# Kernel optimization log

Hardware: AMD Instinct MI355X
Metric: run time of the kernel (lower is better)

The kernel has to match this reference:

```python
import jax, jax.numpy as jnp
import numpy as np

NUM_EMBEDDINGS = 1024
EMBEDDING_DIM = 256

def setup_inputs() -> dict:
    key = jax.random.key(0)
    k1, k2 = jax.random.split(key)
    z_e = jax.random.normal(k1, (32, 256, 64, 64), dtype=jnp.float32)
    # nn.Embedding weight init uniform_(-1/K, 1/K)
    lim = 1.0 / NUM_EMBEDDINGS
    codebook = jax.random.uniform(k2, (NUM_EMBEDDINGS, EMBEDDING_DIM), dtype=jnp.float32,
                                  minval=-lim, maxval=lim)
    return {"z_e": z_e, "codebook": codebook}

def reference(z_e, codebook):
    B, C, H, W = z_e.shape
    # [B,C,H,W] -> [B*H*W, C]
    z_flat = jnp.transpose(z_e, (0, 2, 3, 1)).reshape(-1, C)
    # squared L2 distances: ||z||^2 + ||e||^2 - 2 z.e  -> [N, K]
    distances = (jnp.sum(z_flat ** 2, axis=1, keepdims=True)
                 + jnp.sum(codebook ** 2, axis=1)
                 - 2.0 * jnp.matmul(z_flat, codebook.T))
    encoding_indices = jnp.argmin(distances, axis=1)  # [N]
    z_q = codebook[encoding_indices].reshape(B, H, W, C)
    z_q = jnp.transpose(z_q, (0, 3, 1, 2))  # [B,C,H,W]
    sg = jax.lax.stop_gradient
    codebook_loss = jnp.mean((sg(z_q) - z_e) ** 2)
    commitment_loss = jnp.mean((sg(z_e) - z_q) ** 2)
    return z_q, codebook_loss + 0.25 * commitment_loss, encoding_indices
```

## Files before the change

kernel.cpp:

```cpp
#include <hip/hip_runtime.h>
#include <stdint.h>

typedef __attribute__((ext_vector_type(8))) _Float16 half8;
typedef __attribute__((ext_vector_type(4))) float f32x4;

#define CDIM 256
#define KCODES 1024
#define NPTS 131072
#define ZQ_ELEMS 33554432u
#define CAP 32768
#define MARGIN 3.0e-4f

#define WS_IMG 0
#define WS_S2 (16 * 65536)
#define WS_IDX (WS_S2 + 4096)
#define WS_PART (WS_IDX + NPTS * 4)
#define WS_CNT (WS_PART + 65536)
#define WS_LIST (WS_CNT + 64)

__device__ __forceinline__ float np_pairwise_sq_256(const float* x) {
    float res[2];
#pragma unroll
    for (int h = 0; h < 2; h++) {
        const float* a = x + h * 128;
        float r[8];
#pragma unroll
        for (int j = 0; j < 8; j++) r[j] = __fmul_rn(a[j], a[j]);
#pragma unroll
        for (int i = 8; i < 128; i += 8)
#pragma unroll
            for (int j = 0; j < 8; j++)
                r[j] = __fadd_rn(r[j], __fmul_rn(a[i + j], a[i + j]));
        res[h] = __fadd_rn(__fadd_rn(__fadd_rn(r[0], r[1]), __fadd_rn(r[2], r[3])),
                           __fadd_rn(__fadd_rn(r[4], r[5]), __fadd_rn(r[6], r[7])));
    }
    return __fadd_rn(res[0], res[1]);
}

__global__ __launch_bounds__(256) void vq_prepall(const float* __restrict__ cb,
                                                  unsigned char* __restrict__ img,
                                                  float* __restrict__ s2,
                                                  float* __restrict__ cbT,
                                                  int* __restrict__ cnt) {
    __shared__ float rows[32 * 261];
    int t = threadIdx.x;
    int k0 = blockIdx.x * 32;
    if (blockIdx.x == 0 && t == 0) *cnt = 0;
#pragma unroll
    for (int i = 0; i < 8; i++) {
        int u = i * 256 + t;
        int row = u >> 6, c4 = u & 63;
        float4 v = *(const float4*)&cb[(size_t)(k0 + row) * CDIM + c4 * 4];
        float* d = &rows[row * 261 + c4 * 4];
        d[0] = v.x; d[1] = v.y; d[2] = v.z; d[3] = v.w;
    }
    __syncthreads();
    if (t < 32) s2[k0 + t] = np_pairwise_sq_256(&rows[t * 261]);
#pragma unroll
    for (int i = 0; i < 4; i++) {
        int u = i * 256 + t;
        int cl = u >> 5, cg = u & 31;
        union H { _Float16 h[8]; uint4 u4; } hv;
#pragma unroll
        for (int j = 0; j < 8; j++) hv.h[j] = (_Float16)(rows[cl * 261 + cg * 8 + j] * 1024.f);
        int ks = cg >> 2, l4 = cg & 3;
        int q = cl >> 4, l15 = cl & 15;
        int lane = l4 * 16 + l15;
        *(uint4*)(img + (size_t)blockIdx.x * 16384 + ((ks * 2 + q) << 10) + lane * 16) = hv.u4;
    }
#pragma unroll
    for (int i = 0; i < 32; i++) {
        int u = i * 256 + t;
        int c = u >> 5, row = u & 31;
        cbT[(size_t)c * 1024 + k0 + row] = rows[row * 261 + c];
    }
}

__global__ __launch_bounds__(256, 2) void vq_dist(const float* __restrict__ z,
                                                  const unsigned char* __restrict__ img,
                                                  const float* __restrict__ s2g,
                                                  int* __restrict__ outIdx,
                                                  int* __restrict__ cnt,
                                                  int* __restrict__ list,
                                                  float* __restrict__ partial) {
    __shared__ __align__(16) unsigned char smem[3][16384];
    __shared__ float e2s[1024];
    __shared__ float lred[4];
    int t = threadIdx.x;
    int lane = t & 63, wave = t >> 6;
    int l15 = lane & 15, l4 = lane >> 4;
    int blk0 = blockIdx.x * 256;
    int wbase = blk0 + wave * 64;
    int b = blk0 >> 12;
    int hwb0 = blk0 & 4095;
    const float* zb = z + (size_t)b * (CDIM * 4096);
    unsigned char* sbase = &smem[0][0];

#pragma unroll
    for (int i = 0; i < 4; i++) e2s[t + i * 256] = s2g[t + i * 256];

    half8 aHi[4][8];
    float s1p[4] = {0.f, 0.f, 0.f, 0.f};
#pragma unroll
    for (int ks = 0; ks < 8; ks++) {
        __syncthreads();
#pragma unroll
        for (int i = 0; i < 8; i++) {
            int u = i * 256 + t;
            int row = u >> 6, col16 = u & 63;
            const float* gsrc = zb + (size_t)(ks * 32 + row) * 4096 + hwb0 + col16 * 4;
            __builtin_amdgcn_global_load_lds(
                (const __attribute__((address_space(1))) void*)gsrc,
                (__attribute__((address_space(3))) void*)(sbase + (size_t)u * 16), 16, 0, 0);
        }
        __syncthreads();
#pragma unroll
        for (int m = 0; m < 4; m++) {
            half8 h;
            float ss = s1p[m];
#pragma unroll
            for (int j = 0; j < 8; j++) {
                float f = *(const float*)(sbase +
                        (size_t)(((l4 * 8 + j) << 8) + wave * 64 + m * 16 + l15) * 4) * 32.f;
                h[j] = (_Float16)f;
                ss = fmaf(f, f, ss);
            }
            aHi[m][ks] = h;
            s1p[m] = ss;
        }
    }
    __syncthreads();
#pragma unroll
    for (int m = 0; m < 4; m++) {
        s1p[m] += __shfl_xor(s1p[m], 16);
        s1p[m] += __shfl_xor(s1p[m], 32);
    }

#pragma unroll
    for (int i = 0; i < 4; i++) {
        size_t off = (size_t)(i * 256 + t) * 16;
        __builtin_amdgcn_global_load_lds(
            (const __attribute__((address_space(1))) void*)(img + off),
            (__attribute__((address_space(3))) void*)(&smem[0][0] + off), 16, 0, 0);
    }
#pragma unroll
    for (int i = 0; i < 4; i++) {
        size_t off = (size_t)(i * 256 + t) * 16;
        __builtin_amdgcn_global_load_lds(
            (const __attribute__((address_space(1))) void*)(img + 16384 + off),
            (__attribute__((address_space(3))) void*)(&smem[1][0] + off), 16, 0, 0);
    }

    float bestv[4][4], bestv2[4][4];
    int besti[4][4];
#pragma unroll
    for (int m = 0; m < 4; m++)
#pragma unroll
        for (int j = 0; j < 4; j++) { bestv[m][j] = 3.0e38f; bestv2[m][j] = 3.0e38f; besti[m][j] = 0; }

    int i0 = 0, i1 = 1, i2 = 2;
    for (int chunk = 0; chunk < 32; chunk++) {
        if (chunk < 31) asm volatile("s_waitcnt vmcnt(4)" ::: "memory");
        else            asm volatile("s_waitcnt vmcnt(0)" ::: "memory");
        __builtin_amdgcn_s_barrier();

        if (chunk + 2 < 32) {
            const unsigned char* src = img + (size_t)(chunk + 2) * 16384;
            unsigned char* dst = &smem[0][0] + (size_t)i2 * 16384;
#pragma unroll
            for (int i = 0; i < 4; i++) {
                size_t off = (size_t)(i * 256 + t) * 16;
                __builtin_amdgcn_global_load_lds(
                    (const __attribute__((address_space(1))) void*)(src + off),
                    (__attribute__((address_space(3))) void*)(dst + off), 16, 0, 0);
            }
        }

        f32x4 acc[4][2];
#pragma unroll
        for (int m = 0; m < 4; m++)
#pragma unroll
            for (int q = 0; q < 2; q++) acc[m][q] = (f32x4){0.f, 0.f, 0.f, 0.f};

        const unsigned char* bufc = &smem[0][0] + (size_t)i0 * 16384 + lane * 16;
#pragma unroll
        for (int ks = 0; ks < 8; ks++) {
            half8 b0 = *(const half8*)(bufc + (ks << 11));
            half8 b1 = *(const half8*)(bufc + (ks << 11) + 1024);
#pragma unroll
            for (int m = 0; m < 4; m++) {
                acc[m][0] = __builtin_amdgcn_mfma_f32_16x16x32_f16(aHi[m][ks], b0, acc[m][0], 0, 0, 0);
                acc[m][1] = __builtin_amdgcn_mfma_f32_16x16x32_f16(aHi[m][ks], b1, acc[m][1], 0, 0, 0);
            }
        }
#pragma unroll
        for (int q = 0; q < 2; q++) {
            int code = chunk * 32 + q * 16 + l15;
            float ev = e2s[code];
#pragma unroll
            for (int m = 0; m < 4; m++)
#pragma unroll
                for (int j = 0; j < 4; j++) {
                    float s = fmaf(acc[m][q][j], -6.103515625e-05f, ev);
                    if (s < bestv[m][j]) { bestv2[m][j] = bestv[m][j]; bestv[m][j] = s; besti[m][j] = code; }
                    else if (s < bestv2[m][j]) bestv2[m][j] = s;
                }
        }
        int tmp = i0; i0 = i1; i1 = i2; i2 = tmp;
    }

    float lsum = 0.f;
#pragma unroll
    for (int m = 0; m < 4; m++)
#pragma unroll
        for (int j = 0; j < 4; j++) {
            float v = bestv[m][j], v2 = bestv2[m][j];
            int idx = besti[m][j];
#pragma unroll
            for (int off = 1; off < 16; off <<= 1) {
                float ov = __shfl_xor(v, off);
                float ov2 = __shfl_xor(v2, off);
                int oi = __shfl_xor(idx, off);
                if (ov < v || (ov == v && oi < idx)) { v2 = fminf(v, ov2); v = ov; idx = oi; }
                else v2 = fminf(v2, ov);
            }
            int r = l4 * 4 + j;
            float S1r = __shfl(s1p[m], r) * 9.765625e-4f;
            if (l15 == 0) {
                lsum += S1r + v;
                int p = wbase + m * 16 + l4 * 4 + j;
                outIdx[p] = idx;
                if (v2 - v < MARGIN) {
                    int pos = atomicAdd(cnt, 1);
                    if (pos < CAP) list[pos] = p;
                }
            }
        }
#pragma unroll
    for (int off = 32; off > 0; off >>= 1) lsum += __shfl_down(lsum, off);
    if (lane == 0) lred[wave] = lsum;
    __syncthreads();
    if (t == 0) partial[blockIdx.x] = lred[0] + lred[1] + lred[2] + lred[3];
}

__global__ __launch_bounds__(256) void vq_rescue(const float* __restrict__ z,
                                                 const float* __restrict__ cbT,
                                                 const float* __restrict__ s2,
                                                 const int* __restrict__ list,
                                                 const int* __restrict__ cnt,
                                                 int* __restrict__ outIdx) {
    __shared__ float zs[8][256];
    __shared__ float S1s[8];
    __shared__ float rv[256];
    __shared__ int ri[256];
    int n = *cnt; if (n > CAP) n = CAP;
    int t = threadIdx.x;
    for (int base = blockIdx.x * 8; base < n; base += gridDim.x * 8) {
        int npts = n - base; if (npts > 8) npts = 8;
        __syncthreads();
        {
            int pp = t >> 5, c0 = (t & 31) * 8;
            if (pp < npts) {
                int p = list[base + pp];
                int b = p >> 12, hw = p & 4095;
                const float* zp = z + ((size_t)b << 20) + hw;
#pragma unroll
                for (int j = 0; j < 8; j++) zs[pp][c0 + j] = zp[(size_t)(c0 + j) << 12];
            }
        }
        __syncthreads();
        if (t < npts) S1s[t] = np_pairwise_sq_256(zs[t]);
        __syncthreads();

        float d[8][4];
#pragma unroll
        for (int pp = 0; pp < 8; pp++)
#pragma unroll
            for (int q = 0; q < 4; q++) d[pp][q] = 0.f;
        for (int c = 0; c < 256; c++) {
            const float* er = cbT + c * 1024 + t;
            float e0 = er[0], e1 = er[256], e2v = er[512], e3 = er[768];
#pragma unroll
            for (int pp = 0; pp < 8; pp++) {
                float zc = zs[pp][c];
                d[pp][0] = fmaf(zc, e0, d[pp][0]);
                d[pp][1] = fmaf(zc, e1, d[pp][1]);
                d[pp][2] = fmaf(zc, e2v, d[pp][2]);
                d[pp][3] = fmaf(zc, e3, d[pp][3]);
            }
        }
        float s2v[4] = {s2[t], s2[256 + t], s2[512 + t], s2[768 + t]};

        float bv[8]; int bi[8];
#pragma unroll
        for (int pp = 0; pp < 8; pp++) {
            float v = 3.4e38f; int i0 = 0;
#pragma unroll
            for (int q = 0; q < 4; q++) {
                float dist = __fsub_rn(__fadd_rn(S1s[pp], s2v[q]), __fmul_rn(2.0f, d[pp][q]));
                if (dist < v) { v = dist; i0 = q * 256 + t; }
            }
            bv[pp] = v; bi[pp] = i0;
        }
        for (int pp = 0; pp < 8; pp++) {
            if (pp >= npts) break;
            rv[t] = bv[pp]; ri[t] = bi[pp];
            __syncthreads();
            for (int sft = 128; sft > 0; sft >>= 1) {
                if (t < sft) {
                    if (rv[t + sft] < rv[t] || (rv[t + sft] == rv[t] && ri[t + sft] < ri[t])) {
                        rv[t] = rv[t + sft]; ri[t] = ri[t + sft];
                    }
                }
                __syncthreads();
            }
            if (t == 0) outIdx[list[base + pp]] = ri[0];
            __syncthreads();
        }
    }
}

__global__ __launch_bounds__(256) void vq_gather(const float* __restrict__ cb,
                                                 const int* __restrict__ idxs,
                                                 float* __restrict__ out) {
    int unit = blockIdx.x * 256 + threadIdx.x;
    int hw4 = unit & 1023;
    int cgb = unit >> 10;
    int b = cgb >> 5, cg = cgb & 31;

    int4 ids = *(const int4*)&idxs[(b << 12) + hw4 * 4];
    float va[4][8];
#pragma unroll
    for (int e = 0; e < 4; e++) {
        int id = (e == 0) ? ids.x : (e == 1) ? ids.y : (e == 2) ? ids.z : ids.w;
        const float4* cr = (const float4*)(cb + (size_t)id * CDIM + cg * 8);
        float4 v0 = cr[0], v1 = cr[1];
        va[e][0] = v0.x; va[e][1] = v0.y; va[e][2] = v0.z; va[e][3] = v0.w;
        va[e][4] = v1.x; va[e][5] = v1.y; va[e][6] = v1.z; va[e][7] = v1.w;
    }
#pragma unroll
    for (int j = 0; j < 8; j++) {
        size_t addr = (((size_t)(b * 256 + cg * 8 + j)) << 12) + hw4 * 4;
        float4 ov = {va[0][j], va[1][j], va[2][j], va[3][j]};
        *(float4*)&out[addr] = ov;
    }
    if (cg == 0) {
        size_t ib = (size_t)ZQ_ELEMS + 1u + (b << 12) + hw4 * 4;
        out[ib + 0] = (float)ids.x;
        out[ib + 1] = (float)ids.y;
        out[ib + 2] = (float)ids.z;
        out[ib + 3] = (float)ids.w;
    }
}

__global__ __launch_bounds__(512) void vq_finalize(const float* __restrict__ partial,
                                                   float* __restrict__ out) {
    int t = threadIdx.x;
    double s = (double)partial[t];
#pragma unroll
    for (int off = 32; off > 0; off >>= 1) s += __shfl_down(s, off);
    __shared__ double sd[8];
    if ((t & 63) == 0) sd[t >> 6] = s;
    __syncthreads();
    if (t == 0) {
        double tot = sd[0] + sd[1] + sd[2] + sd[3] + sd[4] + sd[5] + sd[6] + sd[7];
        out[ZQ_ELEMS] = (float)(1.25 * tot / (double)ZQ_ELEMS);
    }
}

extern "C" void kernel_launch(void* const* d_in, const int* in_sizes, int n_in,
                              void* d_out, int out_size, void* d_ws, size_t ws_size,
                              hipStream_t stream) {
    const float* z = (const float*)d_in[0];
    const float* cb = (const float*)d_in[1];
    unsigned char* ws = (unsigned char*)d_ws;
    unsigned char* img = ws + WS_IMG;
    float* s2 = (float*)(ws + WS_S2);
    int* idx = (int*)(ws + WS_IDX);
    float* partial = (float*)(ws + WS_PART);
    int* cnt = (int*)(ws + WS_CNT);
    int* list = (int*)(ws + WS_LIST);
    float* out = (float*)d_out;
    float* cbT = (float*)d_out;

    vq_prepall<<<32, 256, 0, stream>>>(cb, img, s2, cbT, cnt);
    vq_dist<<<512, 256, 0, stream>>>(z, img, s2, idx, cnt, list, partial);
    vq_rescue<<<1024, 256, 0, stream>>>(z, cbT, s2, list, cnt, idx);
    vq_gather<<<4096, 256, 0, stream>>>(cb, idx, out);
    vq_finalize<<<1, 512, 0, stream>>>(partial, out);
}
```

Before: 319.0 us.

## Fuse codebook gather into distance kernel and patch rescued points in place

The separate gather kernel is removed. The distance kernel now writes z_q and the float indices for its 256 points directly, staging codebook rows through shared memory so the NCHW stores are coalesced. The rescue kernel reads the row-major codebook with float4 loads instead of a transposed copy, and it rewrites the z_q column and index only when the refined argmin differs from the first pass. This drops one kernel launch, the transposed-codebook write, and a re-read of the index array. In exchange it adds shared-memory traffic and syncs to vq_dist, and uncoalesced per-point fix-up stores in rescue.

```diff
diff --git a/kernel.cpp b/kernel.cpp
--- a/kernel.cpp
+++ b/kernel.cpp
@@ -40,7 +40,6 @@
 __global__ __launch_bounds__(256) void vq_prepall(const float* __restrict__ cb,
                                                   unsigned char* __restrict__ img,
                                                   float* __restrict__ s2,
-                                                  float* __restrict__ cbT,
                                                   int* __restrict__ cnt) {
     __shared__ float rows[32 * 261];
     int t = threadIdx.x;
@@ -68,24 +67,21 @@
         int lane = l4 * 16 + l15;
         *(uint4*)(img + (size_t)blockIdx.x * 16384 + ((ks * 2 + q) << 10) + lane * 16) = hv.u4;
     }
-#pragma unroll
-    for (int i = 0; i < 32; i++) {
-        int u = i * 256 + t;
-        int c = u >> 5, row = u & 31;
-        cbT[(size_t)c * 1024 + k0 + row] = rows[row * 261 + c];
-    }
 }
 
 __global__ __launch_bounds__(256, 2) void vq_dist(const float* __restrict__ z,
                                                   const unsigned char* __restrict__ img,
                                                   const float* __restrict__ s2g,
+                                                  const float* __restrict__ cb,
                                                   int* __restrict__ outIdx,
                                                   int* __restrict__ cnt,
                                                   int* __restrict__ list,
-                                                  float* __restrict__ partial) {
+                                                  float* __restrict__ partial,
+                                                  float* __restrict__ out) {
     __shared__ __align__(16) unsigned char smem[3][16384];
     __shared__ float e2s[1024];
     __shared__ float lred[4];
+    __shared__ int idxl[256];
     int t = threadIdx.x;
     int lane = t & 63, wave = t >> 6;
     int l15 = lane & 15, l4 = lane >> 4;
@@ -228,7 +224,9 @@
             float S1r = __shfl(s1p[m], r) * 9.765625e-4f;
             if (l15 == 0) {
                 lsum += S1r + v;
-                int p = wbase + m * 16 + l4 * 4 + j;
+                int pl = wave * 64 + m * 16 + l4 * 4 + j;
+                idxl[pl] = idx;
+                int p = blk0 + pl;
                 outIdx[p] = idx;
                 if (v2 - v < MARGIN) {
                     int pos = atomicAdd(cnt, 1);
@@ -236,6 +234,34 @@
                 }
             }
         }
+
+    __syncthreads();
+    out[(size_t)ZQ_ELEMS + 1u + blk0 + t] = (float)idxl[t];
+    int myid = idxl[t];
+    float* tile = (float*)&smem[0][0];
+#pragma unroll 1
+    for (int s = 0; s < 8; s++) {
+        const float4* crow = (const float4*)(cb + (size_t)myid * CDIM + s * 32);
+#pragma unroll
+        for (int i = 0; i < 8; i++) {
+            float4 v = crow[i];
+            int c = i * 4;
+            tile[(c + 0) * 256 + t] = v.x;
+            tile[(c + 1) * 256 + t] = v.y;
+            tile[(c + 2) * 256 + t] = v.z;
+            tile[(c + 3) * 256 + t] = v.w;
+        }
+        __syncthreads();
+#pragma unroll
+        for (int i = 0; i < 8; i++) {
+            int u = i * 256 + t;
+            int row = u >> 6, col4 = u & 63;
+            float4 v = *(const float4*)&tile[row * 256 + col4 * 4];
+            *(float4*)&out[(((size_t)(b * 256 + s * 32 + row)) << 12) + hwb0 + col4 * 4] = v;
+        }
+        __syncthreads();
+    }
+
 #pragma unroll
     for (int off = 32; off > 0; off >>= 1) lsum += __shfl_down(lsum, off);
     if (lane == 0) lred[wave] = lsum;
@@ -244,15 +270,17 @@
 }
 
 __global__ __launch_bounds__(256) void vq_rescue(const float* __restrict__ z,
-                                                 const float* __restrict__ cbT,
+                                                 const float* __restrict__ cb,
                                                  const float* __restrict__ s2,
                                                  const int* __restrict__ list,
                                                  const int* __restrict__ cnt,
-                                                 int* __restrict__ outIdx) {
+                                                 int* __restrict__ outIdx,
+                                                 float* __restrict__ out) {
     __shared__ float zs[8][256];
     __shared__ float S1s[8];
     __shared__ float rv[256];
     __shared__ int ri[256];
+    __shared__ int newbest;
     int n = *cnt; if (n > CAP) n = CAP;
     int t = threadIdx.x;
     for (int base = blockIdx.x * 8; base < n; base += gridDim.x * 8) {
@@ -277,16 +305,22 @@
         for (int pp = 0; pp < 8; pp++)
 #pragma unroll
             for (int q = 0; q < 4; q++) d[pp][q] = 0.f;
-        for (int c = 0; c < 256; c++) {
-            const float* er = cbT + c * 1024 + t;
-            float e0 = er[0], e1 = er[256], e2v = er[512], e3 = er[768];
+        for (int c4 = 0; c4 < 64; c4++) {
+            float4 e[4];
+#pragma unroll
+            for (int q = 0; q < 4; q++)
+                e[q] = *(const float4*)&cb[(size_t)(q * 256 + t) * CDIM + c4 * 4];
 #pragma unroll
             for (int pp = 0; pp < 8; pp++) {
-                float zc = zs[pp][c];
-                d[pp][0] = fmaf(zc, e0, d[pp][0]);
-                d[pp][1] = fmaf(zc, e1, d[pp][1]);
-                d[pp][2] = fmaf(zc, e2v, d[pp][2]);
-                d[pp][3] = fmaf(zc, e3, d[pp][3]);
+                float z0 = zs[pp][c4 * 4 + 0], z1 = zs[pp][c4 * 4 + 1];
+                float z2 = zs[pp][c4 * 4 + 2], z3 = zs[pp][c4 * 4 + 3];
+#pragma unroll
+                for (int q = 0; q < 4; q++) {
+                    d[pp][q] = fmaf(z0, e[q].x, d[pp][q]);
+                    d[pp][q] = fmaf(z1, e[q].y, d[pp][q]);
+                    d[pp][q] = fmaf(z2, e[q].z, d[pp][q]);
+                    d[pp][q] = fmaf(z3, e[q].w, d[pp][q]);
+                }
             }
         }
         float s2v[4] = {s2[t], s2[256 + t], s2[512 + t], s2[768 + t]};
@@ -314,42 +348,23 @@
                 }
                 __syncthreads();
             }
-            if (t == 0) outIdx[list[base + pp]] = ri[0];
+            int p = list[base + pp];
+            if (t == 0) {
+                int old = outIdx[p];
+                newbest = (ri[0] != old) ? ri[0] : -1;
+                if (ri[0] != old) {
+                    outIdx[p] = ri[0];
+                    out[(size_t)ZQ_ELEMS + 1u + p] = (float)ri[0];
+                }
+            }
             __syncthreads();
-        }
-    }
-}
-
-__global__ __launch_bounds__(256) void vq_gather(const float* __restrict__ cb,
-                                                 const int* __restrict__ idxs,
-                                                 float* __restrict__ out) {
-    int unit = blockIdx.x * 256 + threadIdx.x;
-    int hw4 = unit & 1023;
-    int cgb = unit >> 10;
-    int b = cgb >> 5, cg = cgb & 31;
-
-    int4 ids = *(const int4*)&idxs[(b << 12) + hw4 * 4];
-    float va[4][8];
-#pragma unroll
-    for (int e = 0; e < 4; e++) {
-        int id = (e == 0) ? ids.x : (e == 1) ? ids.y : (e == 2) ? ids.z : ids.w;
-        const float4* cr = (const float4*)(cb + (size_t)id * CDIM + cg * 8);
-        float4 v0 = cr[0], v1 = cr[1];
-        va[e][0] = v0.x; va[e][1] = v0.y; va[e][2] = v0.z; va[e][3] = v0.w;
-        va[e][4] = v1.x; va[e][5] = v1.y; va[e][6] = v1.z; va[e][7] = v1.w;
-    }
-#pragma unroll
-    for (int j = 0; j < 8; j++) {
-        size_t addr = (((size_t)(b * 256 + cg * 8 + j)) << 12) + hw4 * 4;
-        float4 ov = {va[0][j], va[1][j], va[2][j], va[3][j]};
-        *(float4*)&out[addr] = ov;
-    }
-    if (cg == 0) {
-        size_t ib = (size_t)ZQ_ELEMS + 1u + (b << 12) + hw4 * 4;
-        out[ib + 0] = (float)ids.x;
-        out[ib + 1] = (float)ids.y;
-        out[ib + 2] = (float)ids.z;
-        out[ib + 3] = (float)ids.w;
+            int nb = newbest;
+            if (nb >= 0) {
+                int b = p >> 12, hw = p & 4095;
+                out[(((size_t)(b * 256 + t)) << 12) + hw] = cb[(size_t)nb * CDIM + t];
+            }
+            __syncthreads();
+        }
     }
 }
 
@@ -381,11 +396,9 @@
     int* cnt = (int*)(ws + WS_CNT);
     int* list = (int*)(ws + WS_LIST);
     float* out = (float*)d_out;
-    float* cbT = (float*)d_out;
-
-    vq_prepall<<<32, 256, 0, stream>>>(cb, img, s2, cbT, cnt);
-    vq_dist<<<512, 256, 0, stream>>>(z, img, s2, idx, cnt, list, partial);
-    vq_rescue<<<1024, 256, 0, stream>>>(z, cbT, s2, list, cnt, idx);
-    vq_gather<<<4096, 256, 0, stream>>>(cb, idx, out);
+
+    vq_prepall<<<32, 256, 0, stream>>>(cb, img, s2, cnt);
+    vq_dist<<<512, 256, 0, stream>>>(z, img, s2, cb, idx, cnt, list, partial, out);
+    vq_rescue<<<1024, 256, 0, stream>>>(z, cb, s2, list, cnt, idx, out);
     vq_finalize<<<1, 512, 0, stream>>>(partial, out);
 }
```

Result: slower. 457.8 us (+43.5%).
